# Kernel optimization log

Hardware: AMD Instinct MI355X
Metric: run time of the kernel (lower is better)

Reference implementation:

```python
import jax, jax.numpy as jnp
import numpy as np

B, C_IN, L = 64, 8, 1024
D, K, E = 64, 256, 512
REG_CH = 0
BETA = 0.25          # EMA-VQ commitment cost
EPS_LIP = 0.01


def _conv1d(x, w, b, stride=1, pad=1):
    # x: [B, Cin, L], w: [Cout, Cin, k] (torch Conv1d layout)
    out = jax.lax.conv_general_dilated(x, w, (stride,), ((pad, pad),),
                                       dimension_numbers=('NCH', 'OIH', 'NCH'))
    return out + b[None, :, None]


def _convT1d(x, w, b, stride=2, pad=1):
    # ConvTranspose1d via input-dilated conv; w: [Cout, Cin, k]
    k = w.shape[-1]
    out = jax.lax.conv_general_dilated(x, w, (1,), ((k - 1 - pad, k - 1 - pad),),
                                       lhs_dilation=(stride,),
                                       dimension_numbers=('NCH', 'OIH', 'NCH'))
    return out + b[None, :, None]


def setup_inputs() -> dict:
    key = jax.random.key(0)
    ks = jax.random.split(key, 12)
    s = 0.05
    return {
        'x': jax.random.uniform(ks[0], (B, C_IN, L), jnp.float32),
        'We1': s * jax.random.normal(ks[1], (64, C_IN, 4), jnp.float32),
        'be1': jnp.zeros((64,), jnp.float32),
        'We2': s * jax.random.normal(ks[2], (128, 64, 4), jnp.float32),
        'be2': jnp.zeros((128,), jnp.float32),
        'We3': s * jax.random.normal(ks[3], (D, 128, 3), jnp.float32),
        'be3': jnp.zeros((D,), jnp.float32),
        'Wd1': s * jax.random.normal(ks[4], (128, D, 4), jnp.float32),
        'bd1': jnp.zeros((128,), jnp.float32),
        'Wd2': s * jax.random.normal(ks[5], (64, 128, 4), jnp.float32),
        'bd2': jnp.zeros((64,), jnp.float32),
        'Wd3': s * jax.random.normal(ks[6], (C_IN, 64, 3), jnp.float32),
        'bd3': jnp.zeros((C_IN,), jnp.float32),
        'codebook': s * jax.random.normal(ks[7], (E, D), jnp.float32),
        'Wlv': s * jax.random.normal(ks[8], (1, 64), jnp.float32),
        'blv': jnp.zeros((1,), jnp.float32),
        'lip_noise': jax.random.normal(ks[9], (B, D, K), jnp.float32),
    }


def reference(x, We1, be1, We2, be2, We3, be3,
              Wd1, bd1, Wd2, bd2, Wd3, bd3,
              codebook, Wlv, blv, lip_noise):
    relu = jax.nn.relu
    # ---- encoder: [B,8,1024] -> z [B,D,K] ----
    h = relu(_conv1d(x, We1, be1, stride=2))          # [B,64,512]
    h = relu(_conv1d(h, We2, be2, stride=2))          # [B,128,256]
    z = _conv1d(h, We3, be3, stride=1)                # [B,D,256]

    # ---- EMA vector quantizer (forward math) ----
    zp = z.transpose(0, 2, 1).reshape(-1, D)          # [B*K, D]
    d2 = (jnp.sum(zp * zp, -1, keepdims=True)
          - 2.0 * zp @ codebook.T
          + jnp.sum(codebook * codebook, -1)[None, :])
    codes = jnp.argmin(d2, axis=-1).reshape(B, K)     # [B,K] int
    zq = codebook[codes].transpose(0, 2, 1)           # [B,D,K]
    vq_loss = BETA * jnp.mean((jax.lax.stop_gradient(zq) - z) ** 2)
    zq = z + jax.lax.stop_gradient(zq - z)            # straight-through

    # ---- decoder (records layer outputs) ----
    def dec(zin):
        h1 = relu(_convT1d(zin, Wd1, bd1))            # [B,128,512]
        h2 = relu(_convT1d(h1, Wd2, bd2))             # [B,64,1024] (injection layer 1)
        yo = _conv1d(h2, Wd3, bd3, stride=1)          # [B,8,1024]
        return yo, h2

    y_raw, h2 = dec(zq)
    y = jax.nn.softmax(y_raw, axis=2)                 # softmax over length dim

    # ---- log-volume regularization branch ----
    lv = jnp.mean(h2, axis=2) @ Wlv.T + blv           # [B,1]
    tgt = jnp.log(jnp.sum(x[:, REG_CH:REG_CH + 1, :], axis=-1, keepdims=True) + 1e-7)  # [B,1,1]
    lv_loss = (tgt - lv) ** 2                         # broadcasts to [B,B,1] (matches torch)

    # ---- decoder Lipschitz loss ----
    y2, _ = dec(zq + EPS_LIP * lip_noise)
    lip = jnp.mean((y_raw - y2) ** 2) / (EPS_LIP ** 2)

    # ---- code reconstruction variance loss ----
    # dist[i,j] = mean over (C,L) of (y_i - y_j)^2  (independent of k in original loop)
    dist = jnp.mean((y[:, None] - y[None, :]) ** 2, axis=(2, 3))        # [B,B]
    same = (codes.T[:, :, None] == codes.T[:, None, :]).astype(y.dtype)  # [K,B,B]
    num = jnp.sum(same * dist[None], axis=(1, 2))                        # [K]
    den = jnp.sum(same, axis=(1, 2)) + 1e-6                              # [K]
    crv = jnp.mean(num / den)

    smoothness = lip + crv
    return (y, lv_loss, vq_loss, smoothness)
```

## Files before the change

### kernel.cpp

```cpp
#include <hip/hip_runtime.h>
#include <float.h>
#include <math.h>

#define DEV_INLINE __device__ __forceinline__


static constexpr size_t F_CN    = 0;
static constexpr size_t F_LVP   = 512;
static constexpr size_t F_TGT   = 768;
static constexpr size_t F_ACC   = 832;
static constexpr size_t F_CODES = 848;
static constexpr size_t F_DIST  = 17232;
static constexpr size_t F_PBEST = 21328;
static constexpr size_t F_PIDX  = 152400;
static constexpr size_t F_SMALL = 283472;

static constexpr size_t A_YRAW = 283472;
static constexpr size_t A_Z2   = 807760;
static constexpr size_t A_H1   = 2904912;
static constexpr size_t A_H2   = 11293520;
static constexpr size_t A_END  = 19682128;

static constexpr size_t B_YRAW = 283472;
static constexpr size_t B_ZQ   = 807760;
static constexpr size_t B_Z    = 1856336;
static constexpr size_t B_H2   = 2904912;
static constexpr size_t B_BIG  = 7099216;
static constexpr size_t B_END  = 11293520;

static constexpr size_t OUT_LV = 524288;

DEV_INLINE float waveReduceSum(float v) {
    #pragma unroll
    for (int m = 32; m > 0; m >>= 1) v += __shfl_xor(v, m, 64);
    return v;
}

DEV_INLINE float blockReduceSum256(float v, float* buf) {
    __syncthreads();
    v = waveReduceSum(v);
    if ((threadIdx.x & 63) == 0) buf[threadIdx.x >> 6] = v;
    __syncthreads();
    return (buf[0] + buf[1]) + (buf[2] + buf[3]);
}

__global__ __launch_bounds__(256)
void preamble_kernel(const float* __restrict__ x, const float* __restrict__ cb,
                     float* __restrict__ cnorm, float* __restrict__ tgt,
                     float* __restrict__ acc) {
    const int blk = blockIdx.x;
    if (blk < 64) {
        __shared__ float red[4];
        const float* __restrict__ xb = x + (size_t)blk * 8 * 1024;
        float s = 0.f;
        for (int t = threadIdx.x; t < 1024; t += 256) s += xb[t];
        const float tot = blockReduceSum256(s, red);
        if (threadIdx.x == 0) tgt[blk] = logf(tot + 1e-7f);
    } else if (blk < 66) {
        const int e = (blk - 64) * 256 + threadIdx.x;
        const float* __restrict__ c = cb + (size_t)e * 64;
        float s = 0.f;
        #pragma unroll
        for (int d = 0; d < 64; ++d) s = fmaf(c[d], c[d], s);
        cnorm[e] = s;
    } else {
        if (threadIdx.x < 16) acc[threadIdx.x] = 0.f;
    }
}

template<int CIN, int LIN, int LOUT, int OG, bool RELU>
__global__ __launch_bounds__(256)
void conv_s2k4(const float* __restrict__ in, const float* __restrict__ w,
               const float* __restrict__ bias, float* __restrict__ out) {
    const int og = blockIdx.x;
    const int b  = blockIdx.y;
    const int t  = blockIdx.z * 256 + threadIdx.x;
    __shared__ __align__(16) float4 wsm[OG * CIN];
    const float4* __restrict__ wg = reinterpret_cast<const float4*>(w) + (size_t)og * OG * CIN;
    for (int idx = threadIdx.x; idx < OG * CIN; idx += 256) wsm[idx] = wg[idx];
    __syncthreads();
    const float* __restrict__ inb = in + (size_t)b * CIN * LIN;
    float acc[OG];
    #pragma unroll
    for (int oo = 0; oo < OG; ++oo) acc[oo] = 0.f;
    const int p0 = 2 * t - 1;
    const bool v0 = (t > 0);
    const bool v3 = (t < LOUT - 1);
    const int q0 = v0 ? p0 : 0;
    const int q3 = v3 ? p0 + 3 : 0;
    for (int i = 0; i < CIN; ++i) {
        const float* __restrict__ row = inb + (size_t)i * LIN;
        float x0 = row[q0]; x0 = v0 ? x0 : 0.f;
        const float x1 = row[p0 + 1];
        const float x2 = row[p0 + 2];
        float x3 = row[q3]; x3 = v3 ? x3 : 0.f;
        #pragma unroll
        for (int oo = 0; oo < OG; ++oo) {
            const float4 wv = wsm[oo * CIN + i];
            acc[oo] = fmaf(x0, wv.x, acc[oo]);
            acc[oo] = fmaf(x1, wv.y, acc[oo]);
            acc[oo] = fmaf(x2, wv.z, acc[oo]);
            acc[oo] = fmaf(x3, wv.w, acc[oo]);
        }
    }
    const int Cout = gridDim.x * OG;
    float* __restrict__ outb = out + ((size_t)b * Cout + og * OG) * LOUT + t;
    #pragma unroll
    for (int oo = 0; oo < OG; ++oo) {
        float v = acc[oo] + bias[og * OG + oo];
        if (RELU) v = fmaxf(v, 0.f);
        outb[(size_t)oo * LOUT] = v;
    }
}

template<int CIN, int LIN, int OG, bool RELU>
__global__ __launch_bounds__(256)
void conv_s1k3(const float* __restrict__ in, const float* __restrict__ w,
               const float* __restrict__ bias, float* __restrict__ out) {
    const int og = blockIdx.x;
    const int b  = blockIdx.y;
    const int t  = blockIdx.z * 256 + threadIdx.x;
    __shared__ __align__(16) float4 wsm[OG * CIN];
    for (int idx = threadIdx.x; idx < OG * CIN; idx += 256) {
        const float* __restrict__ src = w + ((size_t)og * OG * CIN + idx) * 3;
        wsm[idx] = make_float4(src[0], src[1], src[2], 0.f);
    }
    __syncthreads();
    const float* __restrict__ inb = in + (size_t)b * CIN * LIN;
    float acc[OG];
    #pragma unroll
    for (int oo = 0; oo < OG; ++oo) acc[oo] = 0.f;
    const bool vl = (t > 0), vr = (t < LIN - 1);
    const int ql = vl ? t - 1 : 0, qr = vr ? t + 1 : 0;
    for (int i = 0; i < CIN; ++i) {
        const float* __restrict__ row = inb + (size_t)i * LIN;
        float x0 = row[ql]; x0 = vl ? x0 : 0.f;
        const float x1 = row[t];
        float x2 = row[qr]; x2 = vr ? x2 : 0.f;
        #pragma unroll
        for (int oo = 0; oo < OG; ++oo) {
            const float4 wv = wsm[oo * CIN + i];
            acc[oo] = fmaf(x0, wv.x, acc[oo]);
            acc[oo] = fmaf(x1, wv.y, acc[oo]);
            acc[oo] = fmaf(x2, wv.z, acc[oo]);
        }
    }
    const int Cout = gridDim.x * OG;
    float* __restrict__ outb = out + ((size_t)b * Cout + og * OG) * LIN + t;
    #pragma unroll
    for (int oo = 0; oo < OG; ++oo) {
        float v = acc[oo] + bias[og * OG + oo];
        if (RELU) v = fmaxf(v, 0.f);
        outb[(size_t)oo * LIN] = v;
    }
}

template<int CIN, int LIN, int OG, bool RELU>
__global__ __launch_bounds__(256)
void convT_tiled(const float* __restrict__ in, const float* __restrict__ w,
                 const float* __restrict__ bias, float* __restrict__ out) {
    const int og = blockIdx.x;
    const int b  = blockIdx.y;
    const int te = blockIdx.z * 256 + threadIdx.x;
    __shared__ __align__(16) float4 wsm[OG * CIN];
    const float4* __restrict__ wg = reinterpret_cast<const float4*>(w) + (size_t)og * OG * CIN;
    for (int idx = threadIdx.x; idx < OG * CIN; idx += 256) wsm[idx] = wg[idx];
    __syncthreads();
    const float* __restrict__ inb = in + (size_t)b * CIN * LIN;
    float ae[OG], ao[OG];
    #pragma unroll
    for (int oo = 0; oo < OG; ++oo) { ae[oo] = 0.f; ao[oo] = 0.f; }
    const bool vp = (te > 0), vn = (te < LIN - 1);
    const int qp = vp ? te - 1 : 0, qn = vn ? te + 1 : 0;
    for (int i = 0; i < CIN; ++i) {
        const float* __restrict__ row = inb + (size_t)i * LIN;
        float xp = row[qp]; xp = vp ? xp : 0.f;
        const float xc = row[te];
        float xn = row[qn]; xn = vn ? xn : 0.f;
        #pragma unroll
        for (int oo = 0; oo < OG; ++oo) {
            const float4 wv = wsm[oo * CIN + i];
            ae[oo] = fmaf(xp, wv.x, ae[oo]);
            ae[oo] = fmaf(xc, wv.z, ae[oo]);
            ao[oo] = fmaf(xc, wv.y, ao[oo]);
            ao[oo] = fmaf(xn, wv.w, ao[oo]);
        }
    }
    const int Cout = gridDim.x * OG;
    float2* __restrict__ outb =
        reinterpret_cast<float2*>(out + ((size_t)b * Cout + og * OG) * (2 * LIN)) + te;
    #pragma unroll
    for (int oo = 0; oo < OG; ++oo) {
        const float bb = bias[og * OG + oo];
        float ve = ae[oo] + bb, vo = ao[oo] + bb;
        if (RELU) { ve = fmaxf(ve, 0.f); vo = fmaxf(vo, 0.f); }
        outb[(size_t)oo * LIN] = make_float2(ve, vo);
    }
}

__global__ __launch_bounds__(256)
void convd3_both(const float* __restrict__ h2a, const float* __restrict__ h2b,
                 const float* __restrict__ w, const float* __restrict__ bias,
                 float* __restrict__ yraw_out, float* __restrict__ lip_acc) {
    const int b = blockIdx.y;
    const int t = blockIdx.x * 256 + threadIdx.x;
    __shared__ __align__(16) float4 wsm[8 * 64];
    __shared__ float red[4];
    for (int idx = threadIdx.x; idx < 512; idx += 256) {
        const float* __restrict__ src = w + (size_t)idx * 3;
        wsm[idx] = make_float4(src[0], src[1], src[2], 0.f);
    }
    __syncthreads();
    const float* __restrict__ inA = h2a + (size_t)b * 65536;
    const float* __restrict__ inB = h2b + (size_t)b * 65536;
    float accA[8], accB[8];
    #pragma unroll
    for (int oo = 0; oo < 8; ++oo) { accA[oo] = 0.f; accB[oo] = 0.f; }
    const bool vl = (t > 0), vr = (t < 1023);
    const int ql = vl ? t - 1 : 0, qr = vr ? t + 1 : 0;
    for (int i = 0; i < 64; ++i) {
        const float* __restrict__ ra = inA + (size_t)i * 1024;
        const float* __restrict__ rb = inB + (size_t)i * 1024;
        float a0 = ra[ql]; a0 = vl ? a0 : 0.f;
        const float a1 = ra[t];
        float a2 = ra[qr]; a2 = vr ? a2 : 0.f;
        float b0 = rb[ql]; b0 = vl ? b0 : 0.f;
        const float b1 = rb[t];
        float b2 = rb[qr]; b2 = vr ? b2 : 0.f;
        #pragma unroll
        for (int oo = 0; oo < 8; ++oo) {
            const float4 wv = wsm[oo * 64 + i];
            accA[oo] = fmaf(a0, wv.x, accA[oo]);
            accA[oo] = fmaf(a1, wv.y, accA[oo]);
            accA[oo] = fmaf(a2, wv.z, accA[oo]);
            accB[oo] = fmaf(b0, wv.x, accB[oo]);
            accB[oo] = fmaf(b1, wv.y, accB[oo]);
            accB[oo] = fmaf(b2, wv.z, accB[oo]);
        }
    }
    const size_t obase = (size_t)b * 8192 + t;
    float lpart = 0.f;
    #pragma unroll
    for (int oo = 0; oo < 8; ++oo) {
        yraw_out[obase + (size_t)oo * 1024] = accA[oo] + bias[oo];
        const float d = accA[oo] - accB[oo];
        lpart = fmaf(d, d, lpart);
    }
    const float tot = blockReduceSum256(lpart, red);
    if (threadIdx.x == 0) atomicAdd(lip_acc, tot);
}

template<bool LIP>
__global__ __launch_bounds__(256)
void convd3_tiled(const float* __restrict__ in, const float* __restrict__ w,
                  const float* __restrict__ bias, float* __restrict__ yraw_out,
                  const float* __restrict__ yraw_ref, float* __restrict__ lip_acc) {
    const int b = blockIdx.y;
    const int t = blockIdx.x * 256 + threadIdx.x;
    __shared__ __align__(16) float4 wsm[8 * 64];
    __shared__ float red[4];
    for (int idx = threadIdx.x; idx < 512; idx += 256) {
        const float* __restrict__ src = w + (size_t)idx * 3;
        wsm[idx] = make_float4(src[0], src[1], src[2], 0.f);
    }
    __syncthreads();
    const float* __restrict__ inb = in + (size_t)b * 65536;
    float acc[8];
    #pragma unroll
    for (int oo = 0; oo < 8; ++oo) acc[oo] = 0.f;
    const bool vl = (t > 0), vr = (t < 1023);
    const int ql = vl ? t - 1 : 0, qr = vr ? t + 1 : 0;
    for (int i = 0; i < 64; ++i) {
        const float* __restrict__ row = inb + (size_t)i * 1024;
        float x0 = row[ql]; x0 = vl ? x0 : 0.f;
        const float x1 = row[t];
        float x2 = row[qr]; x2 = vr ? x2 : 0.f;
        #pragma unroll
        for (int oo = 0; oo < 8; ++oo) {
            const float4 wv = wsm[oo * 64 + i];
            acc[oo] = fmaf(x0, wv.x, acc[oo]);
            acc[oo] = fmaf(x1, wv.y, acc[oo]);
            acc[oo] = fmaf(x2, wv.z, acc[oo]);
        }
    }
    const size_t obase = (size_t)b * 8192 + t;
    if (!LIP) {
        #pragma unroll
        for (int oo = 0; oo < 8; ++oo)
            yraw_out[obase + (size_t)oo * 1024] = acc[oo] + bias[oo];
    } else {
        float lpart = 0.f;
        #pragma unroll
        for (int oo = 0; oo < 8; ++oo) {
            const float d = (acc[oo] + bias[oo]) - yraw_ref[obase + (size_t)oo * 1024];
            lpart = fmaf(d, d, lpart);
        }
        const float tot = blockReduceSum256(lpart, red);
        if (threadIdx.x == 0) atomicAdd(lip_acc, tot);
    }
}

__global__ __launch_bounds__(256)
void vq_dist_kernel(const float* __restrict__ z, const float* __restrict__ cb,
                    const float* __restrict__ cnorm,
                    float* __restrict__ pbest, int* __restrict__ pidx) {
    const int tile = blockIdx.x;
    const int b = blockIdx.y;
    const int k = threadIdx.x;
    __shared__ __align__(16) float ct[64 * 64];
    __shared__ float cn[64];
    float zr[64];
    #pragma unroll
    for (int d = 0; d < 64; ++d) zr[d] = z[((size_t)(b * 64 + d)) * 256 + k];
    const float* __restrict__ src = cb + (size_t)tile * 64 * 64;
    for (int idx = threadIdx.x; idx < 4096; idx += 256) ct[idx] = src[idx];
    if (threadIdx.x < 64) cn[threadIdx.x] = cnorm[tile * 64 + threadIdx.x];
    __syncthreads();
    float best = FLT_MAX; int bi = 0;
    for (int e = 0; e < 64; ++e) {
        const float4* __restrict__ c4p = reinterpret_cast<const float4*>(ct + e * 64);
        float d0 = 0.f, d1 = 0.f, d2 = 0.f, d3 = 0.f;
        #pragma unroll
        for (int q = 0; q < 16; ++q) {
            const float4 c4 = c4p[q];
            d0 = fmaf(zr[4 * q + 0], c4.x, d0);
            d1 = fmaf(zr[4 * q + 1], c4.y, d1);
            d2 = fmaf(zr[4 * q + 2], c4.z, d2);
            d3 = fmaf(zr[4 * q + 3], c4.w, d3);
        }
        const float dist = cn[e] - 2.f * ((d0 + d1) + (d2 + d3));
        if (dist < best) { best = dist; bi = tile * 64 + e; }
    }
    pbest[((size_t)tile * 64 + b) * 256 + k] = best;
    pidx [((size_t)tile * 64 + b) * 256 + k] = bi;
}

__global__ __launch_bounds__(256)
void vq_combine_kernel(const float* __restrict__ z, const float* __restrict__ cb,
                       const float* __restrict__ pbest, const int* __restrict__ pidx,
                       const float* __restrict__ nz,
                       int* __restrict__ codes, float* __restrict__ zq,
                       float* __restrict__ zq2, float* __restrict__ vq_acc) {
    const int b = blockIdx.x;
    const int k = threadIdx.x;
    __shared__ float red[4];
    float best = FLT_MAX; int bi = 0;
    #pragma unroll
    for (int tile = 0; tile < 8; ++tile) {
        const float v = pbest[((size_t)tile * 64 + b) * 256 + k];
        const int   i = pidx [((size_t)tile * 64 + b) * 256 + k];
        if (v < best) { best = v; bi = i; }
    }
    codes[b * 256 + k] = bi;
    const float* __restrict__ cw = cb + (size_t)bi * 64;
    float part = 0.f;
    #pragma unroll
    for (int d = 0; d < 64; ++d) {
        const size_t loc = ((size_t)(b * 64 + d)) * 256 + k;
        const float c = cw[d];
        const float zv = z[loc];
        zq[loc] = c;
        zq2[loc] = fmaf(0.01f, nz[loc], c);
        const float df = c - zv;
        part = fmaf(df, df, part);
    }
    const float tot = blockReduceSum256(part, red);
    if (threadIdx.x == 0) atomicAdd(vq_acc, tot);
}

__global__ __launch_bounds__(256)
void softmax_kernel(const float* __restrict__ yraw, float* __restrict__ y) {
    const int bc = blockIdx.x;
    const float* __restrict__ r = yraw + (size_t)bc * 1024;
    float* __restrict__ o = y + (size_t)bc * 1024;
    __shared__ float buf[4];
    float v[4];
    float mx = -FLT_MAX;
    #pragma unroll
    for (int j = 0; j < 4; ++j) { v[j] = r[threadIdx.x + 256 * j]; mx = fmaxf(mx, v[j]); }
    #pragma unroll
    for (int m = 32; m > 0; m >>= 1) mx = fmaxf(mx, __shfl_xor(mx, m, 64));
    if ((threadIdx.x & 63) == 0) buf[threadIdx.x >> 6] = mx;
    __syncthreads();
    mx = fmaxf(fmaxf(buf[0], buf[1]), fmaxf(buf[2], buf[3]));
    __syncthreads();
    float e[4]; float s = 0.f;
    #pragma unroll
    for (int j = 0; j < 4; ++j) { e[j] = expf(v[j] - mx); s += e[j]; }
    #pragma unroll
    for (int m = 32; m > 0; m >>= 1) s += __shfl_xor(s, m, 64);
    if ((threadIdx.x & 63) == 0) buf[threadIdx.x >> 6] = s;
    __syncthreads();
    s = (buf[0] + buf[1]) + (buf[2] + buf[3]);
    #pragma unroll
    for (int j = 0; j < 4; ++j) o[threadIdx.x + 256 * j] = e[j] / s;
}

__global__ __launch_bounds__(256)
void lv_kernel(const float* __restrict__ h2, const float* __restrict__ wlv,
               float* __restrict__ lvp) {
    const int b = blockIdx.x, zz = blockIdx.y;
    __shared__ float red[4];
    const float4* __restrict__ hb =
        reinterpret_cast<const float4*>(h2 + (size_t)b * 65536) + (size_t)zz * 4096;
    float s = 0.f;
    for (int i = threadIdx.x; i < 4096; i += 256) {
        const float4 v = hb[i];
        const float wc = wlv[(zz * 4096 + i) >> 8];
        s = fmaf((v.x + v.y) + (v.z + v.w), wc, s);
    }
    const float tot = blockReduceSum256(s, red);
    if (threadIdx.x == 0) lvp[zz * 64 + b] = tot;
}

__global__ __launch_bounds__(256)
void dist_kernel(const float* __restrict__ y, float* __restrict__ dist) {
    const int j = blockIdx.x, i = blockIdx.y;
    if (i > j) return;
    __shared__ float red[4];
    const float4* __restrict__ yi = reinterpret_cast<const float4*>(y + (size_t)i * 8192);
    const float4* __restrict__ yj = reinterpret_cast<const float4*>(y + (size_t)j * 8192);
    float s = 0.f;
    for (int e = threadIdx.x; e < 2048; e += 256) {
        const float4 a = yi[e], c = yj[e];
        const float d0 = a.x - c.x, d1 = a.y - c.y, d2 = a.z - c.z, d3 = a.w - c.w;
        s = fmaf(d0, d0, s); s = fmaf(d1, d1, s);
        s = fmaf(d2, d2, s); s = fmaf(d3, d3, s);
    }
    const float tot = blockReduceSum256(s, red);
    if (threadIdx.x == 0) {
        const float v = tot * (1.f / 8192.f);
        dist[i * 64 + j] = v;
        dist[j * 64 + i] = v;
    }
}

__global__ __launch_bounds__(256)
void crv_kernel(const int* __restrict__ codes, const float* __restrict__ dist,
                float* __restrict__ crv_acc) {
    const int kk = blockIdx.x;
    __shared__ int ck[64];
    __shared__ float red[4];
    if (threadIdx.x < 64) ck[threadIdx.x] = codes[threadIdx.x * 256 + kk];
    __syncthreads();
    float sn = 0.f, sd = 0.f;
    for (int idx = threadIdx.x; idx < 4096; idx += 256) {
        const int i = idx >> 6, j = idx & 63;
        if (ck[i] == ck[j]) { sn += dist[idx]; sd += 1.f; }
    }
    const float tn = blockReduceSum256(sn, red);
    const float td = blockReduceSum256(sd, red);
    if (threadIdx.x == 0) atomicAdd(crv_acc, tn / (td + 1e-6f));
}

__global__ __launch_bounds__(256)
void final_kernel(const float* __restrict__ tgt, const float* __restrict__ lvp,
                  const float* __restrict__ blv, const float* __restrict__ acc,
                  float* __restrict__ out) {
    const int idx = blockIdx.x * 256 + threadIdx.x;
    const int i = idx >> 6, j = idx & 63;
    const float lvj = ((lvp[j] + lvp[64 + j]) + (lvp[128 + j] + lvp[192 + j]))
                      * (1.f / 1024.f) + blv[0];
    const float d = tgt[i] - lvj;
    out[OUT_LV + idx] = d * d;
    if (idx == 0) {
        out[528384] = 0.25f * acc[0] * (1.f / 1048576.f);
        const float lip = acc[1] * (1.f / 524288.f) * 1e4f;
        const float crv = acc[2] * (1.f / 256.f);
        out[528385] = lip + crv;
    }
}

extern "C" void kernel_launch(void* const* d_in, const int* in_sizes, int n_in,
                              void* d_out, int out_size, void* d_ws, size_t ws_size,
                              hipStream_t stream) {
    const float* x   = (const float*)d_in[0];
    const float* We1 = (const float*)d_in[1];
    const float* be1 = (const float*)d_in[2];
    const float* We2 = (const float*)d_in[3];
    const float* be2 = (const float*)d_in[4];
    const float* We3 = (const float*)d_in[5];
    const float* be3 = (const float*)d_in[6];
    const float* Wd1 = (const float*)d_in[7];
    const float* bd1 = (const float*)d_in[8];
    const float* Wd2 = (const float*)d_in[9];
    const float* bd2 = (const float*)d_in[10];
    const float* Wd3 = (const float*)d_in[11];
    const float* bd3 = (const float*)d_in[12];
    const float* cb  = (const float*)d_in[13];
    const float* Wlv = (const float*)d_in[14];
    const float* blv = (const float*)d_in[15];
    const float* nz  = (const float*)d_in[16];
    float* out = (float*)d_out;
    float* ws  = (float*)d_ws;

    float* cnorm = ws + F_CN;
    float* lvp   = ws + F_LVP;
    float* tgt   = ws + F_TGT;
    float* acc   = ws + F_ACC;
    int*   codes = (int*)(ws + F_CODES);
    float* dist  = ws + F_DIST;
    float* pbest = ws + F_PBEST;
    int*   pidx  = (int*)(ws + F_PIDX);

    const bool fused = ws_size >= (size_t)A_END * sizeof(float);

    preamble_kernel<<<67, 256, 0, stream>>>(x, cb, cnorm, tgt, acc);

    if (fused) {
        float* yraw = ws + A_YRAW;
        float* z2   = ws + A_Z2;
        float* h1   = ws + A_H1;
        float* h2   = ws + A_H2;
        float* h1e  = h1;
        float* h2e  = h1 + 2097152;
        float* z    = h2;
        float* zq   = z2;
        float* zq2  = z2 + 1048576;

        conv_s2k4<8, 1024, 512, 8, true><<<dim3(8, 64, 2), 256, 0, stream>>>(x, We1, be1, h1e);
        conv_s2k4<64, 512, 256, 16, true><<<dim3(8, 64, 1), 256, 0, stream>>>(h1e, We2, be2, h2e);
        conv_s1k3<128, 256, 16, false><<<dim3(4, 64, 1), 256, 0, stream>>>(h2e, We3, be3, z);

        vq_dist_kernel<<<dim3(8, 64), 256, 0, stream>>>(z, cb, cnorm, pbest, pidx);
        vq_combine_kernel<<<64, 256, 0, stream>>>(z, cb, pbest, pidx, nz, codes, zq, zq2, &acc[0]);

        convT_tiled<64, 256, 16, true><<<dim3(8, 128, 1), 256, 0, stream>>>(z2, Wd1, bd1, h1);
        convT_tiled<128, 512, 16, true><<<dim3(4, 128, 2), 256, 0, stream>>>(h1, Wd2, bd2, h2);
        lv_kernel<<<dim3(64, 4), 256, 0, stream>>>(h2, Wlv, lvp);
        convd3_both<<<dim3(4, 64), 256, 0, stream>>>(h2, h2 + (size_t)64 * 65536,
                                                     Wd3, bd3, yraw, &acc[1]);
        softmax_kernel<<<512, 256, 0, stream>>>(yraw, out);
    } else {
        float* yraw = ws + B_YRAW;
        float* zq   = ws + B_ZQ;
        float* z    = ws + B_Z;
        float* h2d  = ws + B_H2;
        float* big  = ws + B_BIG;
        float* h1e  = big;
        float* h2e  = big + 2097152;

        conv_s2k4<8, 1024, 512, 8, true><<<dim3(8, 64, 2), 256, 0, stream>>>(x, We1, be1, h1e);
        conv_s2k4<64, 512, 256, 16, true><<<dim3(8, 64, 1), 256, 0, stream>>>(h1e, We2, be2, h2e);
        conv_s1k3<128, 256, 16, false><<<dim3(4, 64, 1), 256, 0, stream>>>(h2e, We3, be3, z);

        vq_dist_kernel<<<dim3(8, 64), 256, 0, stream>>>(z, cb, cnorm, pbest, pidx);
        vq_combine_kernel<<<64, 256, 0, stream>>>(z, cb, pbest, pidx, nz, codes, zq, z, &acc[0]);

        convT_tiled<64, 256, 16, true><<<dim3(8, 64, 1), 256, 0, stream>>>(zq, Wd1, bd1, big);
        convT_tiled<128, 512, 16, true><<<dim3(4, 64, 2), 256, 0, stream>>>(big, Wd2, bd2, h2d);
        convd3_tiled<false><<<dim3(4, 64), 256, 0, stream>>>(h2d, Wd3, bd3, yraw, nullptr, nullptr);
        softmax_kernel<<<512, 256, 0, stream>>>(yraw, out);
        lv_kernel<<<dim3(64, 4), 256, 0, stream>>>(h2d, Wlv, lvp);

        convT_tiled<64, 256, 16, true><<<dim3(8, 64, 1), 256, 0, stream>>>(z, Wd1, bd1, big);
        convT_tiled<128, 512, 16, true><<<dim3(4, 64, 2), 256, 0, stream>>>(big, Wd2, bd2, h2d);
        convd3_tiled<true><<<dim3(4, 64), 256, 0, stream>>>(h2d, Wd3, bd3, nullptr, yraw, &acc[1]);
    }

    dist_kernel<<<dim3(64, 64), 256, 0, stream>>>(out, dist);
    crv_kernel<<<256, 256, 0, stream>>>(codes, dist, &acc[2]);
    final_kernel<<<16, 256, 0, stream>>>(tgt, lvp, blv, acc, out);
}
```

Baseline: 459.3 us.

## Drop LDS weight staging, compute two outputs per thread, split VQ combine

Rewrites every conv and convT kernel to read weights straight from global memory instead of staging them in shared memory. Each thread now computes two or four adjacent outputs so neighbouring inputs are reused, with blocks of 128 threads, output groups of 8 and vectorized stores. It also removes the fused large-workspace path in favour of the sequential two-decoder-pass path, drops shared-memory codebook tiling in vq_dist, and splits vq_combine across four blocks per batch along the D dimension. The aim is to cut LDS traffic and barriers and to raise parallelism, at the cost of more global and scalar-cache weight loads and the loss of the fused decoder path.

```diff
diff --git a/kernel.cpp b/kernel.cpp
--- a/kernel.cpp
+++ b/kernel.cpp
@@ -13,20 +13,12 @@
 static constexpr size_t F_DIST  = 17232;
 static constexpr size_t F_PBEST = 21328;
 static constexpr size_t F_PIDX  = 152400;
-static constexpr size_t F_SMALL = 283472;
-
-static constexpr size_t A_YRAW = 283472;
-static constexpr size_t A_Z2   = 807760;
-static constexpr size_t A_H1   = 2904912;
-static constexpr size_t A_H2   = 11293520;
-static constexpr size_t A_END  = 19682128;
 
 static constexpr size_t B_YRAW = 283472;
 static constexpr size_t B_ZQ   = 807760;
 static constexpr size_t B_Z    = 1856336;
 static constexpr size_t B_H2   = 2904912;
 static constexpr size_t B_BIG  = 7099216;
-static constexpr size_t B_END  = 11293520;
 
 static constexpr size_t OUT_LV = 524288;
 
@@ -69,201 +61,147 @@
 }
 
 template<int CIN, int LIN, int LOUT, int OG, bool RELU>
-__global__ __launch_bounds__(256)
-void conv_s2k4(const float* __restrict__ in, const float* __restrict__ w,
-               const float* __restrict__ bias, float* __restrict__ out) {
+__global__ __launch_bounds__(128)
+void conv_s2k4_sg(const float* __restrict__ in, const float* __restrict__ w,
+                  const float* __restrict__ bias, float* __restrict__ out) {
     const int og = blockIdx.x;
     const int b  = blockIdx.y;
-    const int t  = blockIdx.z * 256 + threadIdx.x;
-    __shared__ __align__(16) float4 wsm[OG * CIN];
+    const int gid = blockIdx.z * 128 + threadIdx.x;
+    const float* __restrict__ inb = in + (size_t)b * CIN * LIN;
     const float4* __restrict__ wg = reinterpret_cast<const float4*>(w) + (size_t)og * OG * CIN;
-    for (int idx = threadIdx.x; idx < OG * CIN; idx += 256) wsm[idx] = wg[idx];
-    __syncthreads();
-    const float* __restrict__ inb = in + (size_t)b * CIN * LIN;
-    float acc[OG];
-    #pragma unroll
-    for (int oo = 0; oo < OG; ++oo) acc[oo] = 0.f;
-    const int p0 = 2 * t - 1;
-    const bool v0 = (t > 0);
-    const bool v3 = (t < LOUT - 1);
-    const int q0 = v0 ? p0 : 0;
-    const int q3 = v3 ? p0 + 3 : 0;
+    float acc0[OG], acc1[OG];
+    #pragma unroll
+    for (int oo = 0; oo < OG; ++oo) { acc0[oo] = 0.f; acc1[oo] = 0.f; }
+    const bool vm = (gid > 0), vp = (gid < LOUT / 2 - 1);
+    const int base = 4 * gid;
+    const int qm = vm ? base - 1 : 0, qp = vp ? base + 4 : 0;
     for (int i = 0; i < CIN; ++i) {
         const float* __restrict__ row = inb + (size_t)i * LIN;
-        float x0 = row[q0]; x0 = v0 ? x0 : 0.f;
-        const float x1 = row[p0 + 1];
-        const float x2 = row[p0 + 2];
-        float x3 = row[q3]; x3 = v3 ? x3 : 0.f;
+        float xm = row[qm]; xm = vm ? xm : 0.f;
+        const float x0 = row[base], x1 = row[base + 1];
+        const float x2 = row[base + 2], x3 = row[base + 3];
+        float xp = row[qp]; xp = vp ? xp : 0.f;
         #pragma unroll
         for (int oo = 0; oo < OG; ++oo) {
-            const float4 wv = wsm[oo * CIN + i];
-            acc[oo] = fmaf(x0, wv.x, acc[oo]);
-            acc[oo] = fmaf(x1, wv.y, acc[oo]);
-            acc[oo] = fmaf(x2, wv.z, acc[oo]);
-            acc[oo] = fmaf(x3, wv.w, acc[oo]);
+            const float4 wv = wg[oo * CIN + i];
+            acc0[oo] = fmaf(xm, wv.x, acc0[oo]);
+            acc0[oo] = fmaf(x0, wv.y, acc0[oo]);
+            acc0[oo] = fmaf(x1, wv.z, acc0[oo]);
+            acc0[oo] = fmaf(x2, wv.w, acc0[oo]);
+            acc1[oo] = fmaf(x1, wv.x, acc1[oo]);
+            acc1[oo] = fmaf(x2, wv.y, acc1[oo]);
+            acc1[oo] = fmaf(x3, wv.z, acc1[oo]);
+            acc1[oo] = fmaf(xp, wv.w, acc1[oo]);
         }
     }
     const int Cout = gridDim.x * OG;
-    float* __restrict__ outb = out + ((size_t)b * Cout + og * OG) * LOUT + t;
     #pragma unroll
     for (int oo = 0; oo < OG; ++oo) {
-        float v = acc[oo] + bias[og * OG + oo];
-        if (RELU) v = fmaxf(v, 0.f);
-        outb[(size_t)oo * LOUT] = v;
+        const float bb = bias[og * OG + oo];
+        float v0 = acc0[oo] + bb, v1 = acc1[oo] + bb;
+        if (RELU) { v0 = fmaxf(v0, 0.f); v1 = fmaxf(v1, 0.f); }
+        reinterpret_cast<float2*>(out + ((size_t)b * Cout + og * OG + oo) * LOUT)[gid] =
+            make_float2(v0, v1);
     }
 }
 
 template<int CIN, int LIN, int OG, bool RELU>
-__global__ __launch_bounds__(256)
-void conv_s1k3(const float* __restrict__ in, const float* __restrict__ w,
-               const float* __restrict__ bias, float* __restrict__ out) {
+__global__ __launch_bounds__(128)
+void conv_s1k3_sg(const float* __restrict__ in, const float* __restrict__ w,
+                  const float* __restrict__ bias, float* __restrict__ out) {
     const int og = blockIdx.x;
     const int b  = blockIdx.y;
-    const int t  = blockIdx.z * 256 + threadIdx.x;
-    __shared__ __align__(16) float4 wsm[OG * CIN];
-    for (int idx = threadIdx.x; idx < OG * CIN; idx += 256) {
-        const float* __restrict__ src = w + ((size_t)og * OG * CIN + idx) * 3;
-        wsm[idx] = make_float4(src[0], src[1], src[2], 0.f);
-    }
-    __syncthreads();
+    const int gid = blockIdx.z * 128 + threadIdx.x;
     const float* __restrict__ inb = in + (size_t)b * CIN * LIN;
-    float acc[OG];
-    #pragma unroll
-    for (int oo = 0; oo < OG; ++oo) acc[oo] = 0.f;
-    const bool vl = (t > 0), vr = (t < LIN - 1);
-    const int ql = vl ? t - 1 : 0, qr = vr ? t + 1 : 0;
+    float acc0[OG], acc1[OG];
+    #pragma unroll
+    for (int oo = 0; oo < OG; ++oo) { acc0[oo] = 0.f; acc1[oo] = 0.f; }
+    const bool vm = (gid > 0), vp = (gid < LIN / 2 - 1);
+    const int t0 = 2 * gid;
+    const int qm = vm ? t0 - 1 : 0, qp = vp ? t0 + 2 : 0;
     for (int i = 0; i < CIN; ++i) {
         const float* __restrict__ row = inb + (size_t)i * LIN;
-        float x0 = row[ql]; x0 = vl ? x0 : 0.f;
-        const float x1 = row[t];
-        float x2 = row[qr]; x2 = vr ? x2 : 0.f;
+        float xm = row[qm]; xm = vm ? xm : 0.f;
+        const float x0 = row[t0], x1 = row[t0 + 1];
+        float xp = row[qp]; xp = vp ? xp : 0.f;
         #pragma unroll
         for (int oo = 0; oo < OG; ++oo) {
-            const float4 wv = wsm[oo * CIN + i];
-            acc[oo] = fmaf(x0, wv.x, acc[oo]);
-            acc[oo] = fmaf(x1, wv.y, acc[oo]);
-            acc[oo] = fmaf(x2, wv.z, acc[oo]);
+            const float* __restrict__ wr = w + ((size_t)(og * OG + oo) * CIN + i) * 3;
+            const float w0 = wr[0], w1 = wr[1], w2 = wr[2];
+            acc0[oo] = fmaf(xm, w0, acc0[oo]);
+            acc0[oo] = fmaf(x0, w1, acc0[oo]);
+            acc0[oo] = fmaf(x1, w2, acc0[oo]);
+            acc1[oo] = fmaf(x0, w0, acc1[oo]);
+            acc1[oo] = fmaf(x1, w1, acc1[oo]);
+            acc1[oo] = fmaf(xp, w2, acc1[oo]);
         }
     }
     const int Cout = gridDim.x * OG;
-    float* __restrict__ outb = out + ((size_t)b * Cout + og * OG) * LIN + t;
     #pragma unroll
     for (int oo = 0; oo < OG; ++oo) {
-        float v = acc[oo] + bias[og * OG + oo];
-        if (RELU) v = fmaxf(v, 0.f);
-        outb[(size_t)oo * LIN] = v;
+        const float bb = bias[og * OG + oo];
+        float v0 = acc0[oo] + bb, v1 = acc1[oo] + bb;
+        if (RELU) { v0 = fmaxf(v0, 0.f); v1 = fmaxf(v1, 0.f); }
+        reinterpret_cast<float2*>(out + ((size_t)b * Cout + og * OG + oo) * LIN)[gid] =
+            make_float2(v0, v1);
     }
 }
 
 template<int CIN, int LIN, int OG, bool RELU>
-__global__ __launch_bounds__(256)
-void convT_tiled(const float* __restrict__ in, const float* __restrict__ w,
-                 const float* __restrict__ bias, float* __restrict__ out) {
+__global__ __launch_bounds__(128)
+void convT_sg(const float* __restrict__ in, const float* __restrict__ w,
+              const float* __restrict__ bias, float* __restrict__ out) {
     const int og = blockIdx.x;
     const int b  = blockIdx.y;
-    const int te = blockIdx.z * 256 + threadIdx.x;
-    __shared__ __align__(16) float4 wsm[OG * CIN];
+    const int gid = blockIdx.z * 128 + threadIdx.x;
+    const int te0 = 2 * gid;
+    const float* __restrict__ inb = in + (size_t)b * CIN * LIN;
     const float4* __restrict__ wg = reinterpret_cast<const float4*>(w) + (size_t)og * OG * CIN;
-    for (int idx = threadIdx.x; idx < OG * CIN; idx += 256) wsm[idx] = wg[idx];
-    __syncthreads();
-    const float* __restrict__ inb = in + (size_t)b * CIN * LIN;
-    float ae[OG], ao[OG];
-    #pragma unroll
-    for (int oo = 0; oo < OG; ++oo) { ae[oo] = 0.f; ao[oo] = 0.f; }
-    const bool vp = (te > 0), vn = (te < LIN - 1);
-    const int qp = vp ? te - 1 : 0, qn = vn ? te + 1 : 0;
+    float a0[OG], a1[OG], a2[OG], a3[OG];
+    #pragma unroll
+    for (int oo = 0; oo < OG; ++oo) { a0[oo] = 0.f; a1[oo] = 0.f; a2[oo] = 0.f; a3[oo] = 0.f; }
+    const bool vm = (gid > 0), vp = (gid < LIN / 2 - 1);
+    const int qm = vm ? te0 - 1 : 0, qp = vp ? te0 + 2 : 0;
     for (int i = 0; i < CIN; ++i) {
         const float* __restrict__ row = inb + (size_t)i * LIN;
+        float xm = row[qm]; xm = vm ? xm : 0.f;
+        const float x0 = row[te0], x1 = row[te0 + 1];
         float xp = row[qp]; xp = vp ? xp : 0.f;
-        const float xc = row[te];
-        float xn = row[qn]; xn = vn ? xn : 0.f;
         #pragma unroll
         for (int oo = 0; oo < OG; ++oo) {
-            const float4 wv = wsm[oo * CIN + i];
-            ae[oo] = fmaf(xp, wv.x, ae[oo]);
-            ae[oo] = fmaf(xc, wv.z, ae[oo]);
-            ao[oo] = fmaf(xc, wv.y, ao[oo]);
-            ao[oo] = fmaf(xn, wv.w, ao[oo]);
+            const float4 wv = wg[oo * CIN + i];
+            a0[oo] = fmaf(xm, wv.x, a0[oo]);
+            a0[oo] = fmaf(x0, wv.z, a0[oo]);
+            a1[oo] = fmaf(x0, wv.y, a1[oo]);
+            a1[oo] = fmaf(x1, wv.w, a1[oo]);
+            a2[oo] = fmaf(x0, wv.x, a2[oo]);
+            a2[oo] = fmaf(x1, wv.z, a2[oo]);
+            a3[oo] = fmaf(x1, wv.y, a3[oo]);
+            a3[oo] = fmaf(xp, wv.w, a3[oo]);
         }
     }
     const int Cout = gridDim.x * OG;
-    float2* __restrict__ outb =
-        reinterpret_cast<float2*>(out + ((size_t)b * Cout + og * OG) * (2 * LIN)) + te;
     #pragma unroll
     for (int oo = 0; oo < OG; ++oo) {
         const float bb = bias[og * OG + oo];
-        float ve = ae[oo] + bb, vo = ao[oo] + bb;
-        if (RELU) { ve = fmaxf(ve, 0.f); vo = fmaxf(vo, 0.f); }
-        outb[(size_t)oo * LIN] = make_float2(ve, vo);
-    }
-}
-
-__global__ __launch_bounds__(256)
-void convd3_both(const float* __restrict__ h2a, const float* __restrict__ h2b,
-                 const float* __restrict__ w, const float* __restrict__ bias,
-                 float* __restrict__ yraw_out, float* __restrict__ lip_acc) {
+        float v0 = a0[oo] + bb, v1 = a1[oo] + bb, v2 = a2[oo] + bb, v3 = a3[oo] + bb;
+        if (RELU) {
+            v0 = fmaxf(v0, 0.f); v1 = fmaxf(v1, 0.f);
+            v2 = fmaxf(v2, 0.f); v3 = fmaxf(v3, 0.f);
+        }
+        reinterpret_cast<float4*>(out + ((size_t)b * Cout + og * OG + oo) * (2 * LIN))[gid] =
+            make_float4(v0, v1, v2, v3);
+    }
+}
+
+template<bool LIP>
+__global__ __launch_bounds__(256)
+void convd3_sg(const float* __restrict__ in, const float* __restrict__ w,
+               const float* __restrict__ bias, float* __restrict__ yraw_out,
+               const float* __restrict__ yraw_ref, float* __restrict__ lip_acc) {
     const int b = blockIdx.y;
     const int t = blockIdx.x * 256 + threadIdx.x;
-    __shared__ __align__(16) float4 wsm[8 * 64];
     __shared__ float red[4];
-    for (int idx = threadIdx.x; idx < 512; idx += 256) {
-        const float* __restrict__ src = w + (size_t)idx * 3;
-        wsm[idx] = make_float4(src[0], src[1], src[2], 0.f);
-    }
-    __syncthreads();
-    const float* __restrict__ inA = h2a + (size_t)b * 65536;
-    const float* __restrict__ inB = h2b + (size_t)b * 65536;
-    float accA[8], accB[8];
-    #pragma unroll
-    for (int oo = 0; oo < 8; ++oo) { accA[oo] = 0.f; accB[oo] = 0.f; }
-    const bool vl = (t > 0), vr = (t < 1023);
-    const int ql = vl ? t - 1 : 0, qr = vr ? t + 1 : 0;
-    for (int i = 0; i < 64; ++i) {
-        const float* __restrict__ ra = inA + (size_t)i * 1024;
-        const float* __restrict__ rb = inB + (size_t)i * 1024;
-        float a0 = ra[ql]; a0 = vl ? a0 : 0.f;
-        const float a1 = ra[t];
-        float a2 = ra[qr]; a2 = vr ? a2 : 0.f;
-        float b0 = rb[ql]; b0 = vl ? b0 : 0.f;
-        const float b1 = rb[t];
-        float b2 = rb[qr]; b2 = vr ? b2 : 0.f;
-        #pragma unroll
-        for (int oo = 0; oo < 8; ++oo) {
-            const float4 wv = wsm[oo * 64 + i];
-            accA[oo] = fmaf(a0, wv.x, accA[oo]);
-            accA[oo] = fmaf(a1, wv.y, accA[oo]);
-            accA[oo] = fmaf(a2, wv.z, accA[oo]);
-            accB[oo] = fmaf(b0, wv.x, accB[oo]);
-            accB[oo] = fmaf(b1, wv.y, accB[oo]);
-            accB[oo] = fmaf(b2, wv.z, accB[oo]);
-        }
-    }
-    const size_t obase = (size_t)b * 8192 + t;
-    float lpart = 0.f;
-    #pragma unroll
-    for (int oo = 0; oo < 8; ++oo) {
-        yraw_out[obase + (size_t)oo * 1024] = accA[oo] + bias[oo];
-        const float d = accA[oo] - accB[oo];
-        lpart = fmaf(d, d, lpart);
-    }
-    const float tot = blockReduceSum256(lpart, red);
-    if (threadIdx.x == 0) atomicAdd(lip_acc, tot);
-}
-
-template<bool LIP>
-__global__ __launch_bounds__(256)
-void convd3_tiled(const float* __restrict__ in, const float* __restrict__ w,
-                  const float* __restrict__ bias, float* __restrict__ yraw_out,
-                  const float* __restrict__ yraw_ref, float* __restrict__ lip_acc) {
-    const int b = blockIdx.y;
-    const int t = blockIdx.x * 256 + threadIdx.x;
-    __shared__ __align__(16) float4 wsm[8 * 64];
-    __shared__ float red[4];
-    for (int idx = threadIdx.x; idx < 512; idx += 256) {
-        const float* __restrict__ src = w + (size_t)idx * 3;
-        wsm[idx] = make_float4(src[0], src[1], src[2], 0.f);
-    }
-    __syncthreads();
     const float* __restrict__ inb = in + (size_t)b * 65536;
     float acc[8];
     #pragma unroll
@@ -277,10 +215,10 @@
         float x2 = row[qr]; x2 = vr ? x2 : 0.f;
         #pragma unroll
         for (int oo = 0; oo < 8; ++oo) {
-            const float4 wv = wsm[oo * 64 + i];
-            acc[oo] = fmaf(x0, wv.x, acc[oo]);
-            acc[oo] = fmaf(x1, wv.y, acc[oo]);
-            acc[oo] = fmaf(x2, wv.z, acc[oo]);
+            const float* __restrict__ wr = w + ((size_t)oo * 64 + i) * 3;
+            acc[oo] = fmaf(x0, wr[0], acc[oo]);
+            acc[oo] = fmaf(x1, wr[1], acc[oo]);
+            acc[oo] = fmaf(x2, wr[2], acc[oo]);
         }
     }
     const size_t obase = (size_t)b * 8192 + t;
@@ -307,28 +245,23 @@
     const int tile = blockIdx.x;
     const int b = blockIdx.y;
     const int k = threadIdx.x;
-    __shared__ __align__(16) float ct[64 * 64];
-    __shared__ float cn[64];
     float zr[64];
     #pragma unroll
     for (int d = 0; d < 64; ++d) zr[d] = z[((size_t)(b * 64 + d)) * 256 + k];
-    const float* __restrict__ src = cb + (size_t)tile * 64 * 64;
-    for (int idx = threadIdx.x; idx < 4096; idx += 256) ct[idx] = src[idx];
-    if (threadIdx.x < 64) cn[threadIdx.x] = cnorm[tile * 64 + threadIdx.x];
-    __syncthreads();
+    const float4* __restrict__ cb4 =
+        reinterpret_cast<const float4*>(cb) + (size_t)tile * 64 * 16;
     float best = FLT_MAX; int bi = 0;
     for (int e = 0; e < 64; ++e) {
-        const float4* __restrict__ c4p = reinterpret_cast<const float4*>(ct + e * 64);
         float d0 = 0.f, d1 = 0.f, d2 = 0.f, d3 = 0.f;
         #pragma unroll
         for (int q = 0; q < 16; ++q) {
-            const float4 c4 = c4p[q];
+            const float4 c4 = cb4[e * 16 + q];
             d0 = fmaf(zr[4 * q + 0], c4.x, d0);
             d1 = fmaf(zr[4 * q + 1], c4.y, d1);
             d2 = fmaf(zr[4 * q + 2], c4.z, d2);
             d3 = fmaf(zr[4 * q + 3], c4.w, d3);
         }
-        const float dist = cn[e] - 2.f * ((d0 + d1) + (d2 + d3));
+        const float dist = cnorm[tile * 64 + e] - 2.f * ((d0 + d1) + (d2 + d3));
         if (dist < best) { best = dist; bi = tile * 64 + e; }
     }
     pbest[((size_t)tile * 64 + b) * 256 + k] = best;
@@ -342,6 +275,7 @@
                        int* __restrict__ codes, float* __restrict__ zq,
                        float* __restrict__ zq2, float* __restrict__ vq_acc) {
     const int b = blockIdx.x;
+    const int dc = blockIdx.y * 16;
     const int k = threadIdx.x;
     __shared__ float red[4];
     float best = FLT_MAX; int bi = 0;
@@ -351,11 +285,12 @@
         const int   i = pidx [((size_t)tile * 64 + b) * 256 + k];
         if (v < best) { best = v; bi = i; }
     }
-    codes[b * 256 + k] = bi;
+    if (blockIdx.y == 0) codes[b * 256 + k] = bi;
     const float* __restrict__ cw = cb + (size_t)bi * 64;
     float part = 0.f;
     #pragma unroll
-    for (int d = 0; d < 64; ++d) {
+    for (int dd = 0; dd < 16; ++dd) {
+        const int d = dc + dd;
         const size_t loc = ((size_t)(b * 64 + d)) * 256 + k;
         const float c = cw[d];
         const float zv = z[loc];
@@ -503,60 +438,33 @@
     float* pbest = ws + F_PBEST;
     int*   pidx  = (int*)(ws + F_PIDX);
 
-    const bool fused = ws_size >= (size_t)A_END * sizeof(float);
+    float* yraw = ws + B_YRAW;
+    float* zq   = ws + B_ZQ;
+    float* z    = ws + B_Z;
+    float* h2d  = ws + B_H2;
+    float* big  = ws + B_BIG;
+    float* h1e  = big;
+    float* h2e  = big + 2097152;
 
     preamble_kernel<<<67, 256, 0, stream>>>(x, cb, cnorm, tgt, acc);
 
-    if (fused) {
-        float* yraw = ws + A_YRAW;
-        float* z2   = ws + A_Z2;
-        float* h1   = ws + A_H1;
-        float* h2   = ws + A_H2;
-        float* h1e  = h1;
-        float* h2e  = h1 + 2097152;
-        float* z    = h2;
-        float* zq   = z2;
-        float* zq2  = z2 + 1048576;
-
-        conv_s2k4<8, 1024, 512, 8, true><<<dim3(8, 64, 2), 256, 0, stream>>>(x, We1, be1, h1e);
-        conv_s2k4<64, 512, 256, 16, true><<<dim3(8, 64, 1), 256, 0, stream>>>(h1e, We2, be2, h2e);
-        conv_s1k3<128, 256, 16, false><<<dim3(4, 64, 1), 256, 0, stream>>>(h2e, We3, be3, z);
-
-        vq_dist_kernel<<<dim3(8, 64), 256, 0, stream>>>(z, cb, cnorm, pbest, pidx);
-        vq_combine_kernel<<<64, 256, 0, stream>>>(z, cb, pbest, pidx, nz, codes, zq, zq2, &acc[0]);
-
-        convT_tiled<64, 256, 16, true><<<dim3(8, 128, 1), 256, 0, stream>>>(z2, Wd1, bd1, h1);
-        convT_tiled<128, 512, 16, true><<<dim3(4, 128, 2), 256, 0, stream>>>(h1, Wd2, bd2, h2);
-        lv_kernel<<<dim3(64, 4), 256, 0, stream>>>(h2, Wlv, lvp);
-        convd3_both<<<dim3(4, 64), 256, 0, stream>>>(h2, h2 + (size_t)64 * 65536,
-                                                     Wd3, bd3, yraw, &acc[1]);
-        softmax_kernel<<<512, 256, 0, stream>>>(yraw, out);
-    } else {
-        float* yraw = ws + B_YRAW;
-        float* zq   = ws + B_ZQ;
-        float* z    = ws + B_Z;
-        float* h2d  = ws + B_H2;
-        float* big  = ws + B_BIG;
-        float* h1e  = big;
-        float* h2e  = big + 2097152;
-
-        conv_s2k4<8, 1024, 512, 8, true><<<dim3(8, 64, 2), 256, 0, stream>>>(x, We1, be1, h1e);
-        conv_s2k4<64, 512, 256, 16, true><<<dim3(8, 64, 1), 256, 0, stream>>>(h1e, We2, be2, h2e);
-        conv_s1k3<128, 256, 16, false><<<dim3(4, 64, 1), 256, 0, stream>>>(h2e, We3, be3, z);
-
-        vq_dist_kernel<<<dim3(8, 64), 256, 0, stream>>>(z, cb, cnorm, pbest, pidx);
-        vq_combine_kernel<<<64, 256, 0, stream>>>(z, cb, pbest, pidx, nz, codes, zq, z, &acc[0]);
-
-        convT_tiled<64, 256, 16, true><<<dim3(8, 64, 1), 256, 0, stream>>>(zq, Wd1, bd1, big);
-        convT_tiled<128, 512, 16, true><<<dim3(4, 64, 2), 256, 0, stream>>>(big, Wd2, bd2, h2d);
-        convd3_tiled<false><<<dim3(4, 64), 256, 0, stream>>>(h2d, Wd3, bd3, yraw, nullptr, nullptr);
-        softmax_kernel<<<512, 256, 0, stream>>>(yraw, out);
-        lv_kernel<<<dim3(64, 4), 256, 0, stream>>>(h2d, Wlv, lvp);
-
-        convT_tiled<64, 256, 16, true><<<dim3(8, 64, 1), 256, 0, stream>>>(z, Wd1, bd1, big);
-        convT_tiled<128, 512, 16, true><<<dim3(4, 64, 2), 256, 0, stream>>>(big, Wd2, bd2, h2d);
-        convd3_tiled<true><<<dim3(4, 64), 256, 0, stream>>>(h2d, Wd3, bd3, nullptr, yraw, &acc[1]);
-    }
+    conv_s2k4_sg<8, 1024, 512, 8, true><<<dim3(8, 64, 2), 128, 0, stream>>>(x, We1, be1, h1e);
+    conv_s2k4_sg<64, 512, 256, 8, true><<<dim3(16, 64, 1), 128, 0, stream>>>(h1e, We2, be2, h2e);
+    conv_s1k3_sg<128, 256, 8, false><<<dim3(8, 64, 1), 128, 0, stream>>>(h2e, We3, be3, z);
+
+    vq_dist_kernel<<<dim3(8, 64), 256, 0, stream>>>(z, cb, cnorm, pbest, pidx);
+    vq_combine_kernel<<<dim3(64, 4), 256, 0, stream>>>(z, cb, pbest, pidx, nz,
+                                                       codes, zq, z, &acc[0]);
+
+    convT_sg<64, 256, 8, true><<<dim3(16, 64, 1), 128, 0, stream>>>(zq, Wd1, bd1, big);
+    convT_sg<128, 512, 8, true><<<dim3(8, 64, 2), 128, 0, stream>>>(big, Wd2, bd2, h2d);
+    convd3_sg<false><<<dim3(4, 64), 256, 0, stream>>>(h2d, Wd3, bd3, yraw, nullptr, nullptr);
+    softmax_kernel<<<512, 256, 0, stream>>>(yraw, out);
+    lv_kernel<<<dim3(64, 4), 256, 0, stream>>>(h2d, Wlv, lvp);
+
+    convT_sg<64, 256, 8, true><<<dim3(16, 64, 1), 128, 0, stream>>>(z, Wd1, bd1, big);
+    convT_sg<128, 512, 8, true><<<dim3(8, 64, 2), 128, 0, stream>>>(big, Wd2, bd2, h2d);
+    convd3_sg<true><<<dim3(4, 64), 256, 0, stream>>>(h2d, Wd3, bd3, nullptr, yraw, &acc[1]);
 
     dist_kernel<<<dim3(64, 64), 256, 0, stream>>>(out, dist);
     crv_kernel<<<256, 256, 0, stream>>>(codes, dist, &acc[2]);
```

Result: no change. 456.8 us (-0.5%).
